# Performance work log

Measured on AMD Instinct MI355X. Metric: run time of the kernel, lower is better.

The kernel has to match this reference:

```python
import jax, jax.numpy as jnp
import numpy as np

NU = 0.5

def _conv3x3(x, w):
    # x: [B,1,Hp,Wp] padded, w: [1,1,3,3]; VALID conv -> [B,1,H,W]
    return jax.lax.conv_general_dilated(
        x, w, window_strides=(1, 1), padding='VALID',
        dimension_numbers=('NCHW', 'OIHW', 'NCHW'))


def setup_inputs() -> dict:
    key = jax.random.key(0)
    k1, k2, k3, k4, k5 = jax.random.split(key, 5)
    B, H, W = 16, 1024, 1024
    u = jax.random.normal(k1, (B, 1, H, W), dtype=jnp.float32)
    u_vel = jax.random.normal(k2, (B, 1, H, W), dtype=jnp.float32)
    w1 = jax.random.normal(k3, (1, 1, 3, 3), dtype=jnp.float32)
    w2 = jax.random.normal(k4, (1, 1, 3, 3), dtype=jnp.float32)
    w3 = jax.random.normal(k5, (1, 1, 3, 3), dtype=jnp.float32)
    return {"u": u, "u_vel": u_vel, "w1": w1, "w2": w2, "w3": w3}


def reference(u, u_vel, w1, w2, w3):
    # replicate pad by 1 on H and W (torch 'replicate' == numpy 'edge')
    u_pad = jnp.pad(u, ((0, 0), (0, 0), (1, 1), (1, 1)), mode='edge')
    Lu = NU * _conv3x3(u_pad, w1) - u_vel * _conv3x3(u_pad, w2) - u_vel * _conv3x3(u_pad, w3)
    return Lu
```

## Files before the change

kernel.cpp:

```cpp
#include <hip/hip_runtime.h>


#define HH 1024
#define WW 1024
#define RPB 8
#define CPW 256
#define NROW (RPB + 2)

__device__ __forceinline__ float rfl(float x) {
    union { float f; int i; } c; c.f = x;
    c.i = __builtin_amdgcn_readfirstlane(c.i);
    return c.f;
}

__global__ __attribute__((amdgpu_flat_work_group_size(64, 64),
                          amdgpu_waves_per_eu(1, 2)))
void burgers_stencil(
    const float* __restrict__ u,
    const float* __restrict__ uvel,
    const float* __restrict__ w1,
    const float* __restrict__ w2,
    const float* __restrict__ w3,
    float* __restrict__ out,
    int rowBlocks, int colBlocks)
{
    const int lane = threadIdx.x;
    int rem = blockIdx.x;
    const int xb = rem % colBlocks; rem /= colBlocks;
    const int yb = rem % rowBlocks; rem /= rowBlocks;
    const int b  = rem;

    const int y0 = yb * RPB;
    const int x0 = xb * CPW + lane * 4;

    const size_t img = (size_t)b * HH * WW;
    const float* ub  = u + img;

    float W1[9], W23[9];
#pragma unroll
    for (int i = 0; i < 9; ++i) {
        W1[i]  = rfl(w1[i]);
        W23[i] = rfl(w2[i] + w3[i]);
    }

    const int xl = (x0 == 0) ? 0 : x0 - 1;
    const int xr = (x0 + 4 >= WW) ? WW - 1 : x0 + 4;

    float4 uv[NROW]; float ul[NROW], ur[NROW];
#pragma unroll
    for (int i = 0; i < NROW; ++i) {
        int yr = y0 - 1 + i;
        yr = yr < 0 ? 0 : (yr > HH - 1 ? HH - 1 : yr);
        const float* row = ub + (size_t)yr * WW;
        uv[i] = *(const float4*)(row + x0);
        ul[i] = row[xl];
        ur[i] = row[xr];
    }
    float4 vv[RPB];
#pragma unroll
    for (int r = 0; r < RPB; ++r)
        vv[r] = *(const float4*)(uvel + img + (size_t)(y0 + r) * WW + x0);

    __builtin_amdgcn_sched_barrier(0);

#pragma unroll
    for (int r = 0; r < RPB; ++r) {
        float p[3][6];
#pragma unroll
        for (int rr = 0; rr < 3; ++rr) {
            const int i = r + rr;
            p[rr][0] = ul[i];
            p[rr][1] = uv[i].x; p[rr][2] = uv[i].y;
            p[rr][3] = uv[i].z; p[rr][4] = uv[i].w;
            p[rr][5] = ur[i];
        }
        const float vel[4] = {vv[r].x, vv[r].y, vv[r].z, vv[r].w};

        float o[4];
#pragma unroll
        for (int j = 0; j < 4; ++j) {
            float c1 = 0.f, c23 = 0.f;
#pragma unroll
            for (int rr = 0; rr < 3; ++rr) {
#pragma unroll
                for (int k = 0; k < 3; ++k) {
                    const float a = p[rr][j + k];
                    c1  = fmaf(W1[rr*3 + k],  a, c1);
                    c23 = fmaf(W23[rr*3 + k], a, c23);
                }
            }
            o[j] = fmaf(-vel[j], c23, 0.5f * c1);
        }
        float4 ov; ov.x = o[0]; ov.y = o[1]; ov.z = o[2]; ov.w = o[3];
        *(float4*)(out + img + (size_t)(y0 + r) * WW + x0) = ov;
    }
}

extern "C" void kernel_launch(void* const* d_in, const int* in_sizes, int n_in,
                              void* d_out, int out_size, void* d_ws, size_t ws_size,
                              hipStream_t stream) {
    const float* u    = (const float*)d_in[0];
    const float* uvel = (const float*)d_in[1];
    const float* w1   = (const float*)d_in[2];
    const float* w2   = (const float*)d_in[3];
    const float* w3   = (const float*)d_in[4];
    float* out        = (float*)d_out;

    const int B = in_sizes[0] / (HH * WW);
    const int rowBlocks = HH / RPB;
    const int colBlocks = WW / CPW;
    dim3 grid(B * rowBlocks * colBlocks);
    dim3 block(64);
    burgers_stencil<<<grid, block, 0, stream>>>(u, uvel, w1, w2, w3, out,
                                                rowBlocks, colBlocks);
}
```

Measured before the change: 174.3 us.

## Share halo columns via wave shuffles, swizzle block order, use nontemporal stores

Replaces the per-lane scalar left/right halo loads with one edge load per row (lanes 0 and 1 fetch the wave's outer halo) plus cross-lane shuffles for the interior neighbours. Workgroup indices are swizzled and decomposed row-block-first so consecutive blocks walk down an image column, which is meant to improve cache reuse of the shared halo rows. Output is written with nontemporal stores to avoid polluting cache, and the waves_per_eu bound is raised. The shuffles add DPP/ds_bpermute work and the swizzle changes DRAM access locality.

Result: slower. 186.7 us (+7.1%).

```diff
diff --git a/kernel.cpp b/kernel.cpp
--- a/kernel.cpp
+++ b/kernel.cpp
@@ -7,6 +7,8 @@
 #define CPW 256
 #define NROW (RPB + 2)
 
+typedef float f32x4 __attribute__((ext_vector_type(4)));
+
 __device__ __forceinline__ float rfl(float x) {
     union { float f; int i; } c; c.f = x;
     c.i = __builtin_amdgcn_readfirstlane(c.i);
@@ -14,7 +16,7 @@
 }
 
 __global__ __attribute__((amdgpu_flat_work_group_size(64, 64),
-                          amdgpu_waves_per_eu(1, 2)))
+                          amdgpu_waves_per_eu(1, 4)))
 void burgers_stencil(
     const float* __restrict__ u,
     const float* __restrict__ uvel,
@@ -25,9 +27,16 @@
     int rowBlocks, int colBlocks)
 {
     const int lane = threadIdx.x;
-    int rem = blockIdx.x;
+
+    const int nwg = gridDim.x;
+    int swz = blockIdx.x;
+    if ((nwg & 7) == 0) {
+        const int chunk = nwg >> 3;
+        swz = (swz & 7) * chunk + (swz >> 3);
+    }
+    int rem = swz;
+    const int yb = rem % rowBlocks; rem /= rowBlocks;
     const int xb = rem % colBlocks; rem /= colBlocks;
-    const int yb = rem % rowBlocks; rem /= rowBlocks;
     const int b  = rem;
 
     const int y0 = yb * RPB;
@@ -43,18 +52,19 @@
         W23[i] = rfl(w2[i] + w3[i]);
     }
 
-    const int xl = (x0 == 0) ? 0 : x0 - 1;
-    const int xr = (x0 + 4 >= WW) ? WW - 1 : x0 + 4;
+    const int xleft = xb * CPW;
+    const int xeL = (xleft == 0) ? 0 : xleft - 1;
+    const int xeR = (xleft + CPW >= WW) ? WW - 1 : xleft + CPW;
+    const int xe  = (lane & 1) ? xeR : xeL;
 
-    float4 uv[NROW]; float ul[NROW], ur[NROW];
+    float4 uv[NROW]; float ev[NROW];
 #pragma unroll
     for (int i = 0; i < NROW; ++i) {
         int yr = y0 - 1 + i;
         yr = yr < 0 ? 0 : (yr > HH - 1 ? HH - 1 : yr);
         const float* row = ub + (size_t)yr * WW;
         uv[i] = *(const float4*)(row + x0);
-        ul[i] = row[xl];
-        ur[i] = row[xr];
+        ev[i] = row[xe];
     }
     float4 vv[RPB];
 #pragma unroll
@@ -62,6 +72,17 @@
         vv[r] = *(const float4*)(uvel + img + (size_t)(y0 + r) * WW + x0);
 
     __builtin_amdgcn_sched_barrier(0);
+
+    float ul[NROW], ur[NROW];
+#pragma unroll
+    for (int i = 0; i < NROW; ++i) {
+        const float eL = __shfl(ev[i], 0);
+        const float eR = __shfl(ev[i], 1);
+        const float fl = __shfl_up(uv[i].w, 1);
+        const float fr = __shfl_down(uv[i].x, 1);
+        ul[i] = (lane == 0)  ? eL : fl;
+        ur[i] = (lane == 63) ? eR : fr;
+    }
 
 #pragma unroll
     for (int r = 0; r < RPB; ++r) {
@@ -91,8 +112,9 @@
             }
             o[j] = fmaf(-vel[j], c23, 0.5f * c1);
         }
-        float4 ov; ov.x = o[0]; ov.y = o[1]; ov.z = o[2]; ov.w = o[3];
-        *(float4*)(out + img + (size_t)(y0 + r) * WW + x0) = ov;
+        f32x4 ov; ov.x = o[0]; ov.y = o[1]; ov.z = o[2]; ov.w = o[3];
+        __builtin_nontemporal_store(
+            ov, (f32x4*)(out + img + (size_t)(y0 + r) * WW + x0));
     }
 }
 
```

## Use full-row 256-thread blocks with rolling prefetch and XCD swizzle

Applied to the files above, without the earlier changes.

Each block now covers a full 1024-wide row band of 8 rows with 256 threads, instead of one 64-thread wave per 256-column segment. The neighbour columns are no longer fetched as scalar loads; each row is covered by two overlapping float4 loads. The u and u_vel rows move through rotating register buffers, with the next row prefetched while the current one is computed, in place of loading every row up front. A block-index swizzle groups consecutive bands per XCD to improve L2 locality, at the cost of somewhat more load traffic from the overlapping loads.

Result: slower. 193.7 us (+11.1%).

```diff
diff --git a/kernel.cpp b/kernel.cpp
--- a/kernel.cpp
+++ b/kernel.cpp
@@ -3,9 +3,10 @@
 
 #define HH 1024
 #define WW 1024
-#define RPB 8
-#define CPW 256
-#define NROW (RPB + 2)
+#define ROWS 8
+#define TPB 256
+
+typedef float f32x4 __attribute__((ext_vector_type(4)));
 
 __device__ __forceinline__ float rfl(float x) {
     union { float f; int i; } c; c.f = x;
@@ -13,8 +14,8 @@
     return c.f;
 }
 
-__global__ __attribute__((amdgpu_flat_work_group_size(64, 64),
-                          amdgpu_waves_per_eu(1, 2)))
+__global__ __attribute__((amdgpu_flat_work_group_size(TPB, TPB),
+                          amdgpu_waves_per_eu(4, 8)))
 void burgers_stencil(
     const float* __restrict__ u,
     const float* __restrict__ uvel,
@@ -22,19 +23,23 @@
     const float* __restrict__ w2,
     const float* __restrict__ w3,
     float* __restrict__ out,
-    int rowBlocks, int colBlocks)
+    int bandsPerImg)
 {
-    const int lane = threadIdx.x;
-    int rem = blockIdx.x;
-    const int xb = rem % colBlocks; rem /= colBlocks;
-    const int yb = rem % rowBlocks; rem /= rowBlocks;
-    const int b  = rem;
+    int swz = blockIdx.x;
+    const int nwg = gridDim.x;
+    if ((nwg & 7) == 0) {
+        const int chunk = nwg >> 3;
+        swz = (swz & 7) * chunk + (swz >> 3);
+    }
+    const int band = swz % bandsPerImg;
+    const int b    = swz / bandsPerImg;
+    const int y0   = band * ROWS;
+    const int x0   = (int)threadIdx.x * 4;
 
-    const int y0 = yb * RPB;
-    const int x0 = xb * CPW + lane * 4;
-
-    const size_t img = (size_t)b * HH * WW;
-    const float* ub  = u + img;
+    const size_t img = (size_t)b * (HH * WW);
+    const float* ub = u + img;
+    const float* vb = uvel + img;
+    float* ob       = out + img;
 
     float W1[9], W23[9];
 #pragma unroll
@@ -43,38 +48,51 @@
         W23[i] = rfl(w2[i] + w3[i]);
     }
 
-    const int xl = (x0 == 0) ? 0 : x0 - 1;
-    const int xr = (x0 + 4 >= WW) ? WW - 1 : x0 + 4;
+    const bool le = (x0 == 0);
+    const bool re = (x0 + 4 >= WW);
+    const int  ca = le ? 0 : x0 - 1;
+    const int  cb = re ? WW - 4 : x0 + 1;
 
-    float4 uv[NROW]; float ul[NROW], ur[NROW];
+    float4 ua[5], ubv[5];
 #pragma unroll
-    for (int i = 0; i < NROW; ++i) {
+    for (int i = 0; i < 4; ++i) {
         int yr = y0 - 1 + i;
         yr = yr < 0 ? 0 : (yr > HH - 1 ? HH - 1 : yr);
         const float* row = ub + (size_t)yr * WW;
-        uv[i] = *(const float4*)(row + x0);
-        ul[i] = row[xl];
-        ur[i] = row[xr];
+        ua[i]  = *(const float4*)(row + ca);
+        ubv[i] = *(const float4*)(row + cb);
     }
-    float4 vv[RPB];
+    float4 vl[4];
 #pragma unroll
-    for (int r = 0; r < RPB; ++r)
-        vv[r] = *(const float4*)(uvel + img + (size_t)(y0 + r) * WW + x0);
-
-    __builtin_amdgcn_sched_barrier(0);
+    for (int i = 0; i < 3; ++i) {
+        int yr = y0 + i; yr = yr > HH - 1 ? HH - 1 : yr;
+        vl[i] = *(const float4*)(vb + (size_t)yr * WW + x0);
+    }
 
 #pragma unroll
-    for (int r = 0; r < RPB; ++r) {
+    for (int r = 0; r < ROWS; ++r) {
+        {
+            int pf = y0 + r + 3; pf = pf > HH - 1 ? HH - 1 : pf;
+            const float* prow = ub + (size_t)pf * WW;
+            ua[(r + 4) % 5]  = *(const float4*)(prow + ca);
+            ubv[(r + 4) % 5] = *(const float4*)(prow + cb);
+            vl[(r + 3) % 4]  = *(const float4*)(vb + (size_t)pf * WW + x0);
+        }
+
         float p[3][6];
 #pragma unroll
         for (int rr = 0; rr < 3; ++rr) {
-            const int i = r + rr;
-            p[rr][0] = ul[i];
-            p[rr][1] = uv[i].x; p[rr][2] = uv[i].y;
-            p[rr][3] = uv[i].z; p[rr][4] = uv[i].w;
-            p[rr][5] = ur[i];
+            const float4 a  = ua[(r + rr) % 5];
+            const float4 bq = ubv[(r + rr) % 5];
+            p[rr][0] = a.x;
+            p[rr][1] = le ? a.x : a.y;
+            p[rr][2] = le ? a.y : a.z;
+            p[rr][3] = le ? a.z : a.w;
+            p[rr][4] = le ? a.w : (re ? bq.w : bq.z);
+            p[rr][5] = bq.w;
         }
-        const float vel[4] = {vv[r].x, vv[r].y, vv[r].z, vv[r].w};
+        const float4 vv = vl[r % 4];
+        const float vel[4] = {vv.x, vv.y, vv.z, vv.w};
 
         float o[4];
 #pragma unroll
@@ -92,7 +110,7 @@
             o[j] = fmaf(-vel[j], c23, 0.5f * c1);
         }
         float4 ov; ov.x = o[0]; ov.y = o[1]; ov.z = o[2]; ov.w = o[3];
-        *(float4*)(out + img + (size_t)(y0 + r) * WW + x0) = ov;
+        *(float4*)(ob + (size_t)(y0 + r) * WW + x0) = ov;
     }
 }
 
@@ -107,10 +125,9 @@
     float* out        = (float*)d_out;
 
     const int B = in_sizes[0] / (HH * WW);
-    const int rowBlocks = HH / RPB;
-    const int colBlocks = WW / CPW;
-    dim3 grid(B * rowBlocks * colBlocks);
-    dim3 block(64);
+    const int bandsPerImg = HH / ROWS;
+    dim3 grid(B * bandsPerImg);
+    dim3 block(TPB);
     burgers_stencil<<<grid, block, 0, stream>>>(u, uvel, w1, w2, w3, out,
-                                                rowBlocks, colBlocks);
+                                                bandsPerImg);
 }
```
